# Optimization experiments

Hardware: AMD Instinct MI355X
Metric: run time of the kernel (lower is better)

The kernel has to match this reference:

```python
import jax, jax.numpy as jnp
import numpy as np

B, T, D, H, C, M = 128, 96, 256, 256, 8, 64
COMB = 4 * D + H  # z, z_prime, x_i, global_dynamics, h


def setup_inputs() -> dict:
    key = jax.random.key(0)
    ks = jax.random.split(key, 24)
    X = jax.random.normal(ks[0], (B, T, D), jnp.float32)
    X_last = jax.random.normal(ks[1], (B, T, D), jnp.float32)
    Mask = jax.random.bernoulli(ks[2], 0.5, (B, T, D)).astype(jnp.float32)
    Delta = jax.random.uniform(ks[3], (B, T, D), jnp.float32, 0.0, 5.0)
    X_last_b = jax.random.normal(ks[4], (B, T, D), jnp.float32)
    Delta_b = jax.random.uniform(ks[5], (B, T, D), jnp.float32, 0.0, 5.0)
    x = jnp.stack([X, X_last, Mask, Delta, X_last_b, Delta_b], axis=1)  # [B,6,T,D]
    X_mean = jax.random.normal(ks[6], (1, T, D), jnp.float32)
    clusters = jax.random.randint(ks[7], (D,), 1, C + 1, jnp.int64)
    s = 1.0 / np.sqrt(COMB)
    def U(k, shape, sc):
        return jax.random.uniform(k, shape, jnp.float32, -sc, sc)
    params = {
        'W_i': U(ks[8], (H, COMB), s), 'b_i': U(ks[9], (H,), s),
        'W_f': U(ks[10], (H, COMB), s), 'b_f': U(ks[11], (H,), s),
        'W_o': U(ks[12], (H, COMB), s), 'b_o': U(ks[13], (H,), s),
        'W_c': U(ks[14], (H, COMB), s), 'b_c': U(ks[15], (H,), s),
        'W_fc': U(ks[16], (D, H), 1.0 / np.sqrt(H)), 'b_fc': U(ks[17], (D,), 1.0 / np.sqrt(H)),
        'gz_w': U(ks[18], (D,), 1.0 / np.sqrt(D)), 'gz_b': U(ks[19], (D,), 1.0 / np.sqrt(D)),
        'gzp_w': U(ks[20], (D,), 1.0 / np.sqrt(D)), 'gzp_b': U(ks[21], (D,), 1.0 / np.sqrt(D)),
        'memory': jax.random.uniform(ks[22], (C, M, D), jnp.float32, -1.0 / np.sqrt(M), 1.0 / np.sqrt(M)),
    }
    k2 = jax.random.split(ks[23], 2)
    params['local_w'] = jax.random.uniform(k2[0], (3, D), jnp.float32, -1.0 / np.sqrt(3.0), 1.0 / np.sqrt(3.0))
    params['global_w'] = jax.random.uniform(k2[1], (C,), jnp.float32, -1.0 / np.sqrt(C), 1.0 / np.sqrt(C))
    return dict(x=x, X_mean=X_mean, clusters=clusters, **params)


def reference(x, X_mean, clusters, W_i, b_i, W_f, b_f, W_o, b_o, W_c, b_c,
              W_fc, b_fc, gz_w, gz_b, gzp_w, gzp_b, memory, local_w, global_w):
    # cluster one-hot feature masks: [C, D] (cluster ids are 1-based)
    cmask = (clusters[None, :] == jnp.arange(1, C + 1, dtype=clusters.dtype)[:, None]).astype(x.dtype)

    X, X_last, Mask, Delta, X_last_b, Delta_b = [x[:, i] for i in range(6)]  # each [B,T,D]
    xm = X_mean[0]  # [T,D]

    def step(carry, inp):
        h, c = carry
        xt, xl, xlb, m, d, db, mean = inp
        # FilterLinear with eye filter == diagonal linear; GRU-D decay
        dz = jnp.exp(-jax.nn.relu(d * gz_w + gz_b))
        dzp = jnp.exp(-jax.nn.relu(db * gzp_w + gzp_b))
        z = m * xt + (1 - m) * (dz * xl + (1 - dz) * mean)
        zp = m * xt + (1 - m) * (dzp * xlb + (1 - dzp) * mean)
        x_i = h @ W_fc.T + b_fc  # [B,D]
        local_stats = local_w[0] * z + local_w[1] * zp + local_w[2] * x_i  # [B,D]
        # per-cluster masked local stats -> memory attention
        li = local_stats[:, None, :] * cmask[None]              # [B,C,D]
        scores = jnp.einsum('cmd,bcd->bcm', memory, li)          # [B,C,M]
        s = jax.nn.softmax(scores, axis=-1)
        gd = jnp.einsum('bcm,cmd->bcd', s, memory)               # [B,C,D]
        gd = jnp.einsum('bcd,c->bd', gd, global_w)               # [B,D]
        combined = jnp.concatenate([z, zp, x_i, gd, h], axis=1)  # [B,4D+H]
        i = jax.nn.sigmoid(combined @ W_i.T + b_i)
        f = jax.nn.sigmoid(combined @ W_f.T + b_f)
        o = jax.nn.sigmoid(combined @ W_o.T + b_o)
        ct = jnp.tanh(combined @ W_c.T + b_c)
        c = f * c + i * ct
        h = o * jnp.tanh(c)
        out = h @ W_fc.T + b_fc
        return (h, c), out

    h0 = jnp.zeros((x.shape[0], H), x.dtype)
    c0 = jnp.zeros((x.shape[0], H), x.dtype)
    xs = (X.transpose(1, 0, 2), X_last.transpose(1, 0, 2), X_last_b.transpose(1, 0, 2),
          Mask.transpose(1, 0, 2), Delta.transpose(1, 0, 2), Delta_b.transpose(1, 0, 2), xm)
    _, outs = jax.lax.scan(step, (h0, c0), xs)
    return outs.transpose(1, 0, 2)  # [B,T,D]
```

## Files before the change

kernel.cpp:

```cpp
#include <hip/hip_runtime.h>
#include <hip/hip_bf16.h>
#include <hip/hip_fp16.h>
#include <cstdint>
#include <cstddef>


#define PLANE 24576
#define GRP 16

using bf16_t = __hip_bfloat16;
typedef __bf16 bf16x8 __attribute__((ext_vector_type(8)));
typedef float  f32x4  __attribute__((ext_vector_type(4)));
typedef unsigned int u32x4 __attribute__((ext_vector_type(4)));

__device__ __forceinline__ float  b2f(bf16_t v){ return __bfloat162float(v); }
__device__ __forceinline__ bf16_t f2b(float v){ return __float2bfloat16(v); }
__device__ __forceinline__ float ldF(const void* p, size_t i, int f32){
  return f32 ? ((const float*)p)[i] : b2f(((const bf16_t*)p)[i]);
}
__device__ __forceinline__ bf16x8 ld_frag(const void* p){
  union { uint4 u; bf16x8 v; } c;
  c.u = *(const uint4*)p;
  return c.v;
}
__device__ __forceinline__ f32x4 mfma_bf16(bf16x8 a, bf16x8 b, f32x4 c){
  return __builtin_amdgcn_mfma_f32_16x16x32_bf16(a, b, c, 0, 0, 0);
}

__device__ __forceinline__ u32x4 ld_cg(const void* p){
  u32x4 r;
  asm volatile("global_load_dwordx4 %0, %1, off sc0 sc1"
               : "=v"(r) : "v"(p) : "memory");
  return r;
}
__device__ __forceinline__ void st_cg(void* p, u32x4 v){
  asm volatile("global_store_dwordx4 %0, %1, off sc0 sc1"
               :: "v"(p), "v"(v) : "memory");
}
__device__ __forceinline__ int ld_flag(const int* p){
  int r;
  asm volatile("global_load_dword %0, %1, off sc0 sc1\n\ts_waitcnt vmcnt(0)"
               : "=v"(r) : "v"(p) : "memory");
  return r;
}
__device__ __forceinline__ void vm_wait0(){
  asm volatile("s_waitcnt vmcnt(0)" ::: "memory");
  __builtin_amdgcn_sched_barrier(0);
}

__global__ __launch_bounds__(64) void k_detect(
    const uint32_t* __restrict__ xu, const uint32_t* __restrict__ clu,
    int* __restrict__ flags)
{
  __shared__ int cnt[2];
  int t = threadIdx.x;
  if (t < 2) cnt[t] = 0;
  __syncthreads();
  uint32_t v = xu[2*PLANE + t];
  if (v == 0u || v == 0x3F800000u) atomicAdd(&cnt[0], 1);
  if (clu[2*t + 1] == 0u) atomicAdd(&cnt[1], 1);
  __syncthreads();
  if (t == 0){
    flags[0] = (cnt[0] >= 48) ? 1 : 0;
    flags[1] = (cnt[1] >= 60) ? 1 : 0;
  }
}

__global__ __launch_bounds__(256) void k_zero(int* __restrict__ bar){
  bar[threadIdx.x] = 0;
}

__global__ __launch_bounds__(256) void k_canon(
    const void* __restrict__ Wfc, const void* __restrict__ Xmean,
    const void* __restrict__ bfc, const void* __restrict__ localw,
    const void* __restrict__ globalw, const void* __restrict__ gzw,
    const void* __restrict__ gzb, const void* __restrict__ gzpw,
    const void* __restrict__ gzpb, const int* __restrict__ flags,
    bf16_t* __restrict__ WfcC, bf16_t* __restrict__ XmC,
    bf16_t* __restrict__ bfcC, bf16_t* __restrict__ lwC,
    bf16_t* __restrict__ gwC, float* __restrict__ gzC)
{
  const int f32 = flags[0];
  int i = blockIdx.x*256 + threadIdx.x;
  if (i < 65536) WfcC[i] = f2b(ldF(Wfc, i, f32));
  if (i < 24576) XmC[i]  = f2b(ldF(Xmean, i, f32));
  if (i < 256)   bfcC[i] = f2b(ldF(bfc, i, f32));
  if (i < 768)   lwC[i]  = f2b(ldF(localw, i, f32));
  if (i < 8)     gwC[i]  = f2b(ldF(globalw, i, f32));
  if (i < 256){
    gzC[i]       = ldF(gzw,  i, f32);
    gzC[256 + i] = ldF(gzb,  i, f32);
    gzC[512 + i] = ldF(gzpw, i, f32);
    gzC[768 + i] = ldF(gzpb, i, f32);
  }
}

__global__ __launch_bounds__(256) void k_fold(
    const void* __restrict__ Wi, const void* __restrict__ Wf,
    const void* __restrict__ Wo, const void* __restrict__ Wc,
    const void* __restrict__ bi, const void* __restrict__ bfg,
    const void* __restrict__ bo, const void* __restrict__ bcg,
    const void* __restrict__ Wfc, const void* __restrict__ bfc,
    const int* __restrict__ flags,
    bf16_t* __restrict__ U, bf16_t* __restrict__ Uz, float* __restrict__ bias2)
{
  const int f32 = flags[0];
  int n = blockIdx.x; int g = n & 3; int j = n >> 2;
  const void* Wg = (g==0)?Wi:(g==1)?Wf:(g==2)?Wo:Wc;
  const void* bg = (g==0)?bi:(g==1)?bfg:(g==2)?bo:bcg;
  const size_t wb = (size_t)j*1280;
  int k = threadIdx.x;
  float acc = 0.f;
  for (int d=0; d<256; ++d)
    acc += ldF(Wg, wb+512+d, f32) * ldF(Wfc, (size_t)d*256+k, f32);
  U[(size_t)n*512 + k]        = f2b(acc + ldF(Wg, wb+1024+k, f32));
  U[(size_t)n*512 + 256 + k]  = f2b(ldF(Wg, wb+768+k, f32));
  Uz[(size_t)n*512 + k]       = f2b(ldF(Wg, wb+k, f32));
  Uz[(size_t)n*512 + 256 + k] = f2b(ldF(Wg, wb+256+k, f32));
  __shared__ float red[256];
  red[k] = ldF(Wg, wb+512+k, f32) * ldF(bfc, k, f32);
  __syncthreads();
  for (int s=128; s>0; s>>=1){ if (k<s) red[k]+=red[k+s]; __syncthreads(); }
  if (k==0) bias2[n] = red[0] + ldF(bg, j, f32);
}

__global__ __launch_bounds__(256) void k_foldG(
    const void* __restrict__ Wi, const void* __restrict__ Wf,
    const void* __restrict__ Wo, const void* __restrict__ Wc,
    const void* __restrict__ memory, const int* __restrict__ flags,
    bf16_t* __restrict__ G)
{
  const int f32 = flags[0];
  __shared__ float wrow[4][256];
  int j = blockIdx.x; int tid = threadIdx.x;
  const void* Wg[4] = {Wi,Wf,Wo,Wc};
  for (int g=0; g<4; ++g)
    wrow[g][tid] = ldF(Wg[g], (size_t)j*1280 + 768 + tid, f32);
  __syncthreads();
  for (int half=0; half<2; ++half){
    int cm = half*256 + tid;
    float a0=0,a1=0,a2=0,a3=0;
    for (int d=0; d<256; ++d){
      float mv = ldF(memory, (size_t)cm*256 + d, f32);
      a0 += wrow[0][d]*mv; a1 += wrow[1][d]*mv;
      a2 += wrow[2][d]*mv; a3 += wrow[3][d]*mv;
    }
    G[(size_t)(4*j+0)*512 + cm] = f2b(a0);
    G[(size_t)(4*j+1)*512 + cm] = f2b(a1);
    G[(size_t)(4*j+2)*512 + cm] = f2b(a2);
    G[(size_t)(4*j+3)*512 + cm] = f2b(a3);
  }
}

__global__ __launch_bounds__(256) void k_foldQ(
    const int* __restrict__ clusters, const void* __restrict__ memory,
    const bf16_t* __restrict__ lwC, const bf16_t* __restrict__ WfcC,
    const bf16_t* __restrict__ bfcC, const int* __restrict__ flags,
    bf16_t* __restrict__ Mem2, bf16_t* __restrict__ Qbf, float* __restrict__ qb)
{
  const int f32 = flags[0], i64 = flags[1];
  const int cm = blockIdx.x; const int c = cm >> 6;
  const int tid = threadIdx.x;
  __shared__ float ml2[256];
  __shared__ float red[256];
  int cv = i64 ? clusters[2*tid] : clusters[tid];
  float mv = (cv == c+1) ? ldF(memory, (size_t)cm*256 + tid, f32) : 0.f;
  Mem2[(size_t)cm*256 + tid] = f2b(mv);
  float m2 = mv * b2f(lwC[512 + tid]);
  ml2[tid] = m2;
  red[tid] = m2 * b2f(bfcC[tid]);
  __syncthreads();
  float acc = 0.f;
  for (int d=0; d<256; ++d)
    acc += ml2[d] * b2f(WfcC[(size_t)d*256 + tid]);
  Qbf[(size_t)cm*256 + tid] = f2b(acc);
  for (int s=128; s>0; s>>=1){ if (tid<s) red[tid]+=red[tid+s]; __syncthreads(); }
  if (tid==0) qb[cm] = red[0];
}

__global__ __launch_bounds__(256) void k_zzp(
    const void* __restrict__ x, const bf16_t* __restrict__ XmC,
    const float* __restrict__ gzC, const bf16_t* __restrict__ lwC,
    const int* __restrict__ flags,
    bf16_t* __restrict__ Zcat, bf16_t* __restrict__ Zl)
{
  const int f32 = flags[0];
  int r = blockIdx.x;
  int t = r >> 7, b = r & 127, d = threadIdx.x;
  size_t base = (size_t)b*6*PLANE + (size_t)t*256 + d;
  float xt = ldF(x, base          , f32);
  float xl = ldF(x, base +   PLANE, f32);
  float mk = ldF(x, base + 2*PLANE, f32);
  float de = ldF(x, base + 3*PLANE, f32);
  float xlb= ldF(x, base + 4*PLANE, f32);
  float deb= ldF(x, base + 5*PLANE, f32);
  float mean = b2f(XmC[t*256+d]);
  float dz  = expf(-fmaxf(0.f, de *gzC[d]     + gzC[256+d]));
  float dzp = expf(-fmaxf(0.f, deb*gzC[512+d] + gzC[768+d]));
  float z  = mk*xt + (1.f-mk)*(dz *xl  + (1.f-dz )*mean);
  float zp = mk*xt + (1.f-mk)*(dzp*xlb + (1.f-dzp)*mean);
  Zcat[(size_t)r*512 + d]       = f2b(z);
  Zcat[(size_t)r*512 + 256 + d] = f2b(zp);
  Zl[(size_t)r*256 + d] = f2b(b2f(lwC[d])*z + b2f(lwC[256+d])*zp);
}

__global__ __launch_bounds__(256) void k_zc(
    const bf16_t* __restrict__ Zcat, const bf16_t* __restrict__ Uz,
    const float* __restrict__ bias2, __half* __restrict__ zc)
{
  const int tid = threadIdx.x;
  const int w = tid>>6, l = tid&63, q=l>>4, cl=l&15;
  const int mq = w&1, nq = w>>1;
  const int m0 = blockIdx.x*128, n0 = blockIdx.y*128;
  f32x4 acc[4][4];
#pragma unroll
  for (int a=0;a<4;++a)
#pragma unroll
    for (int b2=0;b2<4;++b2) acc[a][b2] = (f32x4){0.f,0.f,0.f,0.f};
  for (int ks=0; ks<16; ++ks){
    bf16x8 av[4], bv[4];
#pragma unroll
    for (int mi=0;mi<4;++mi)
      av[mi] = ld_frag(&Zcat[(size_t)(m0+mq*64+mi*16+cl)*512 + ks*32 + q*8]);
#pragma unroll
    for (int ni=0;ni<4;++ni)
      bv[ni] = ld_frag(&Uz[(size_t)(n0+nq*64+ni*16+cl)*512 + ks*32 + q*8]);
#pragma unroll
    for (int mi=0;mi<4;++mi)
#pragma unroll
      for (int ni=0;ni<4;++ni)
        acc[mi][ni] = mfma_bf16(av[mi], bv[ni], acc[mi][ni]);
  }
#pragma unroll
  for (int mi=0;mi<4;++mi)
#pragma unroll
    for (int ni=0;ni<4;++ni)
#pragma unroll
      for (int rr=0;rr<4;++rr){
        int m = m0 + mq*64 + mi*16 + q*4 + rr;
        int n = n0 + nq*64 + ni*16 + cl;
        zc[(size_t)m*1024 + n] = __float2half(acc[mi][ni][rr] + bias2[n]);
      }
}

__global__ __launch_bounds__(256) void k_szm(
    const bf16_t* __restrict__ Zl, const bf16_t* __restrict__ Mem2,
    const float* __restrict__ qb, __half* __restrict__ SzM)
{
  const int tid = threadIdx.x;
  const int w = tid>>6, l = tid&63, q=l>>4, cl=l&15;
  const int mq = w&1, nq = w>>1;
  const int m0 = blockIdx.x*128, n0 = blockIdx.y*128;
  f32x4 acc[4][4];
#pragma unroll
  for (int a=0;a<4;++a)
#pragma unroll
    for (int b2=0;b2<4;++b2) acc[a][b2] = (f32x4){0.f,0.f,0.f,0.f};
  for (int ks=0; ks<8; ++ks){
    bf16x8 av[4], bv[4];
#pragma unroll
    for (int mi=0;mi<4;++mi)
      av[mi] = ld_frag(&Zl[(size_t)(m0+mq*64+mi*16+cl)*256 + ks*32 + q*8]);
#pragma unroll
    for (int ni=0;ni<4;++ni)
      bv[ni] = ld_frag(&Mem2[(size_t)(n0+nq*64+ni*16+cl)*256 + ks*32 + q*8]);
#pragma unroll
    for (int mi=0;mi<4;++mi)
#pragma unroll
      for (int ni=0;ni<4;++ni)
        acc[mi][ni] = mfma_bf16(av[mi], bv[ni], acc[mi][ni]);
  }
#pragma unroll
  for (int mi=0;mi<4;++mi)
#pragma unroll
    for (int ni=0;ni<4;++ni)
#pragma unroll
      for (int rr=0;rr<4;++rr){
        int m = m0 + mq*64 + mi*16 + q*4 + rr;
        int n = n0 + nq*64 + ni*16 + cl;
        SzM[(size_t)m*512 + n] = __float2half(acc[mi][ni][rr] + qb[n]);
      }
}

__global__ __launch_bounds__(256) void k_out(
    const bf16_t* __restrict__ hSeq, const bf16_t* __restrict__ WfcC,
    const bf16_t* __restrict__ bfcC, const int* __restrict__ flags,
    void* __restrict__ outv)
{
  const int f32 = flags[0];
  const int tid = threadIdx.x;
  const int w = tid>>6, l = tid&63, q=l>>4, cl=l&15;
  const int mq = w&1, nq = w>>1;
  const int m0 = blockIdx.x*128, n0 = blockIdx.y*128;
  f32x4 acc[4][4];
#pragma unroll
  for (int a=0;a<4;++a)
#pragma unroll
    for (int b2=0;b2<4;++b2) acc[a][b2] = (f32x4){0.f,0.f,0.f,0.f};
  for (int ks=0; ks<8; ++ks){
    bf16x8 av[4], bv[4];
#pragma unroll
    for (int mi=0;mi<4;++mi)
      av[mi] = ld_frag(&hSeq[(size_t)(128 + m0+mq*64+mi*16+cl)*256 + ks*32 + q*8]);
#pragma unroll
    for (int ni=0;ni<4;++ni)
      bv[ni] = ld_frag(&WfcC[(size_t)(n0+nq*64+ni*16+cl)*256 + ks*32 + q*8]);
#pragma unroll
    for (int mi=0;mi<4;++mi)
#pragma unroll
      for (int ni=0;ni<4;++ni)
        acc[mi][ni] = mfma_bf16(av[mi], bv[ni], acc[mi][ni]);
  }
#pragma unroll
  for (int mi=0;mi<4;++mi)
#pragma unroll
    for (int ni=0;ni<4;++ni)
#pragma unroll
      for (int rr=0;rr<4;++rr){
        int m = m0 + mq*64 + mi*16 + q*4 + rr;
        int n = n0 + nq*64 + ni*16 + cl;
        float v = acc[mi][ni][rr] + b2f(bfcC[n]);
        int b = m & 127, tt = m >> 7;
        size_t ob = ((size_t)b*96 + tt)*256 + n;
        if (f32) ((float*)outv)[ob] = v; else ((bf16_t*)outv)[ob] = f2b(v);
      }
}

__global__ __launch_bounds__(256) void k_main(
    const bf16_t* __restrict__ gwC,
    const bf16_t* __restrict__ U, const bf16_t* __restrict__ G,
    const bf16_t* __restrict__ Qbf,
    const __half* __restrict__ zc, const __half* __restrict__ SzM,
    bf16_t* __restrict__ hSeq, bf16_t* __restrict__ tSeq,
    int* __restrict__ bar)
{
  __shared__ bf16_t Us[64][264];
  __shared__ bf16_t Gs[64][520];
  __shared__ bf16_t Qs[64][264];
  __shared__ bf16_t hS[16][264];
  __shared__ bf16_t tS[16][520];
  __shared__ bf16_t hO[16][16];
  __shared__ bf16_t tO[16][64];
  __shared__ float redmx[4][16];
  __shared__ float redsm[4][16];

  const int tid = threadIdx.x;
  const int W = tid>>6, l = tid&63, q = l>>4, cl = l&15;
  const int g = blockIdx.x & 7, s = blockIdx.x >> 3;
  const int r0 = g*16;
  const int n0 = s*64;
  int* barp = bar + g*32;

  for (int i=tid; i<64*32; i+=256){ int r=i>>5, c8=(i&31)*8;
    *(uint4*)(&Us[r][c8]) = *(const uint4*)(U + (size_t)(n0+r)*512 + c8); }
  for (int i=tid; i<64*64; i+=256){ int r=i>>6, c8=(i&63)*8;
    *(uint4*)(&Gs[r][c8]) = *(const uint4*)(G + (size_t)(n0+r)*512 + c8); }
  if (s<8)
    for (int i=tid; i<64*32; i+=256){ int r=i>>5, c8=(i&31)*8;
      *(uint4*)(&Qs[r][c8]) = *(const uint4*)(Qbf + (size_t)(s*64+r)*256 + c8); }
  for (int i=tid; i<16*264; i+=256) hS[i/264][i%264] = f2b(0.f);
  const float gw_c = (s<8)? b2f(gwC[s]) : 0.f;
  float creg[4] = {0.f,0.f,0.f,0.f};
  __syncthreads();

  for (int t=0; t<96; ++t){
    f32x4 acc;
#pragma unroll
    for (int rr=0; rr<4; ++rr)
      acc[rr] = __half2float(zc[((size_t)(t*128)+r0+q*4+rr)*1024 + n0 + W*16 + cl]);
    f32x4 sa = {0.f,0.f,0.f,0.f};
    if (s<8){
#pragma unroll
      for (int rr=0; rr<4; ++rr)
        sa[rr] = __half2float(SzM[((size_t)(t*128)+r0+q*4+rr)*512 + s*64 + W*16 + cl]);
    }
    if (t>0){
      if (tid==0){ while (ld_flag(barp+0) < GRP*t) {} }
      __syncthreads();
      const bf16_t* hsrc = hSeq + (size_t)t*128*256;
      u32x4 a0 = ld_cg(hsrc + (size_t)(r0 + (tid>>5))*256 + (tid&31)*8);
      u32x4 a1 = ld_cg(hsrc + (size_t)(r0 + 8 + (tid>>5))*256 + (tid&31)*8);
      vm_wait0();
      *(u32x4*)(&hS[tid>>5][(tid&31)*8]) = a0;
      *(u32x4*)(&hS[8 + (tid>>5)][(tid&31)*8]) = a1;
      __syncthreads();
    }
    if (s<8){
#pragma unroll
      for (int ks=0; ks<8; ++ks){
        bf16x8 a = ld_frag(&hS[cl][ks*32 + q*8]);
        bf16x8 b = ld_frag(&Qs[W*16+cl][ks*32 + q*8]);
        sa = mfma_bf16(a, b, sa);
      }
#pragma unroll
      for (int rr=0; rr<4; ++rr){
        float m = sa[rr];
        m = fmaxf(m, __shfl_xor(m,1));
        m = fmaxf(m, __shfl_xor(m,2));
        m = fmaxf(m, __shfl_xor(m,4));
        m = fmaxf(m, __shfl_xor(m,8));
        if (cl==0) redmx[W][q*4+rr] = m;
      }
      __syncthreads();
      float e4[4];
#pragma unroll
      for (int rr=0; rr<4; ++rr){
        int row = q*4+rr;
        float mx = fmaxf(fmaxf(redmx[0][row],redmx[1][row]),
                         fmaxf(redmx[2][row],redmx[3][row]));
        float e = expf(sa[rr]-mx);
        e4[rr] = e;
        float ss = e;
        ss += __shfl_xor(ss,1); ss += __shfl_xor(ss,2);
        ss += __shfl_xor(ss,4); ss += __shfl_xor(ss,8);
        if (cl==0) redsm[W][row] = ss;
      }
      __syncthreads();
#pragma unroll
      for (int rr=0; rr<4; ++rr){
        int row = q*4+rr;
        float sm = redsm[0][row]+redsm[1][row]+redsm[2][row]+redsm[3][row];
        tO[row][W*16 + cl] = f2b(e4[rr]*gw_c/sm);
      }
      __syncthreads();
      if (tid < 128){
        int r = tid>>3, c8 = (tid&7)*8;
        u32x4 v = *(u32x4*)(&tO[r][c8]);
        st_cg(tSeq + (size_t)t*128*512 + (size_t)(r0+r)*512 + s*64 + c8, v);
      }
      vm_wait0();
      __syncthreads();
      if (tid==0) atomicAdd(barp+16, 1);
    }
#pragma unroll
    for (int ks=0; ks<8; ++ks){
      bf16x8 a = ld_frag(&hS[cl][ks*32 + q*8]);
      bf16x8 b = ld_frag(&Us[W*16+cl][ks*32 + q*8]);
      acc = mfma_bf16(a, b, acc);
    }
    if (tid==0){ while (ld_flag(barp+16) < 8*(t+1)) {} }
    __syncthreads();
    {
      const bf16_t* tsrc = tSeq + (size_t)t*128*512;
      u32x4 b0 = ld_cg(tsrc + (size_t)(r0 + (tid>>6)     )*512 + (tid&63)*8);
      u32x4 b1 = ld_cg(tsrc + (size_t)(r0 + (tid>>6) +  4)*512 + (tid&63)*8);
      u32x4 b2 = ld_cg(tsrc + (size_t)(r0 + (tid>>6) +  8)*512 + (tid&63)*8);
      u32x4 b3 = ld_cg(tsrc + (size_t)(r0 + (tid>>6) + 12)*512 + (tid&63)*8);
      vm_wait0();
      *(u32x4*)(&tS[(tid>>6)     ][(tid&63)*8]) = b0;
      *(u32x4*)(&tS[(tid>>6) +  4][(tid&63)*8]) = b1;
      *(u32x4*)(&tS[(tid>>6) +  8][(tid&63)*8]) = b2;
      *(u32x4*)(&tS[(tid>>6) + 12][(tid&63)*8]) = b3;
      __syncthreads();
    }
#pragma unroll
    for (int ks=0; ks<16; ++ks){
      bf16x8 a = ld_frag(&tS[cl][ks*32 + q*8]);
      bf16x8 b = ld_frag(&Gs[W*16+cl][ks*32 + q*8]);
      acc = mfma_bf16(a, b, acc);
    }
    const int base = l & ~3;
#pragma unroll
    for (int rr=0; rr<4; ++rr){
      float p = acc[rr];
      float pi = __shfl(p, base+0);
      float pf = __shfl(p, base+1);
      float po = __shfl(p, base+2);
      float pc = __shfl(p, base+3);
      float iv = 1.f/(1.f+expf(-pi));
      float fv = 1.f/(1.f+expf(-pf));
      float ov = 1.f/(1.f+expf(-po));
      float cv = tanhf(pc);
      float cn = fv*creg[rr] + iv*cv;
      creg[rr] = cn;
      float hv = ov * tanhf(cn);
      if ((l&3)==0)
        hO[q*4+rr][W*4 + (cl>>2)] = f2b(hv);
    }
    __syncthreads();
    if (tid < 32){
      int r = tid>>1, c8 = (tid&1)*8;
      u32x4 v = *(u32x4*)(&hO[r][c8]);
      st_cg(hSeq + (size_t)(t+1)*128*256 + (size_t)(r0+r)*256 + s*16 + c8, v);
    }
    vm_wait0();
    __syncthreads();
    if (tid==0) atomicAdd(barp+0, 1);
  }
}

extern "C" void kernel_launch(void* const* d_in, const int* in_sizes, int n_in,
                              void* d_out, int out_size, void* d_ws, size_t ws_size,
                              hipStream_t stream)
{
  const void* x       = d_in[0];
  const void* Xmean   = d_in[1];
  const int*  clusters= (const int*)d_in[2];
  const void* Wi  = d_in[3];
  const void* bi  = d_in[4];
  const void* Wf  = d_in[5];
  const void* bfp = d_in[6];
  const void* Wo  = d_in[7];
  const void* bo  = d_in[8];
  const void* Wc  = d_in[9];
  const void* bcp = d_in[10];
  const void* Wfc = d_in[11];
  const void* bfc = d_in[12];
  const void* gzw = d_in[13];
  const void* gzb = d_in[14];
  const void* gzpw= d_in[15];
  const void* gzpb= d_in[16];
  const void* memory = d_in[17];
  const void* localw = d_in[18];
  const void* globalw= d_in[19];
  (void)in_sizes; (void)n_in; (void)out_size; (void)ws_size;

  char* ws = (char*)d_ws;
  size_t off = 0;
  auto take = [&](size_t bytes)->char*{
    char* p = ws + off; off = (off + bytes + 255) & ~(size_t)255; return p; };
  int*    flags  = (int*)   take(16);
  int*    bar    = (int*)   take(256*4);
  bf16_t* U      = (bf16_t*)take((size_t)1024*512*2);
  bf16_t* Uz     = (bf16_t*)take((size_t)1024*512*2);
  bf16_t* G      = (bf16_t*)take((size_t)1024*512*2);
  bf16_t* WfcC   = (bf16_t*)take((size_t)65536*2);
  bf16_t* XmC    = (bf16_t*)take((size_t)24576*2);
  bf16_t* bfcC   = (bf16_t*)take(256*2);
  bf16_t* lwC    = (bf16_t*)take(768*2);
  bf16_t* gwC    = (bf16_t*)take(8*2);
  float*  gzC    = (float*) take(1024*4);
  float*  bias2  = (float*) take(1024*4);
  bf16_t* Mem2   = (bf16_t*)take((size_t)512*256*2);
  bf16_t* Qbf    = (bf16_t*)take((size_t)512*256*2);
  float*  qb     = (float*) take(512*4);
  __half* zc     = (__half*)take((size_t)12288*1024*2);
  __half* SzM    = (__half*)take((size_t)12288*512*2);
  char* bigA = take((size_t)12288*512*2);
  char* bigB = take((size_t)97*128*256*2);
  bf16_t* Zcat = (bf16_t*)bigA;
  bf16_t* tSeq = (bf16_t*)bigA;
  bf16_t* Zl   = (bf16_t*)bigB;
  bf16_t* hSeq = (bf16_t*)bigB;

  k_detect<<<1,    64, 0,stream>>>((const uint32_t*)x, (const uint32_t*)clusters, flags);
  k_zero  <<<1,    256,0,stream>>>(bar);
  k_canon <<<256,  256,0,stream>>>(Wfc, Xmean, bfc, localw, globalw,
                                   gzw, gzb, gzpw, gzpb, flags,
                                   WfcC, XmC, bfcC, lwC, gwC, gzC);
  k_fold  <<<1024, 256,0,stream>>>(Wi,Wf,Wo,Wc, bi,bfp,bo,bcp, Wfc,bfc, flags,
                                   U, Uz, bias2);
  k_foldG <<<256,  256,0,stream>>>(Wi,Wf,Wo,Wc, memory, flags, G);
  k_foldQ <<<512,  256,0,stream>>>(clusters, memory, lwC, WfcC, bfcC, flags,
                                   Mem2, Qbf, qb);
  k_zzp   <<<12288,256,0,stream>>>(x, XmC, gzC, lwC, flags, Zcat, Zl);
  k_zc    <<<dim3(96,8),256,0,stream>>>(Zcat, Uz, bias2, zc);
  k_szm   <<<dim3(96,4),256,0,stream>>>(Zl, Mem2, qb, SzM);
  k_main  <<<128,  256,0,stream>>>(gwC, U, G, Qbf, zc, SzM, hSeq, tSeq, bar);
  k_out   <<<dim3(96,2),256,0,stream>>>(hSeq, WfcC, bfcC, flags, d_out);
}
```

Before: 1.047 ms.

## Replace block barriers and atomic counters with per-wave flag sync in recurrent kernel

The persistent recurrent kernel drops its shared-memory staging and __syncthreads-based step synchronisation. Each wave now polls an array of per-wave step flags (one flag per producer wave) and loads h and softmax-weight fragments straight from global memory into registers for the MFMAs. The memory-attention softmax is computed by a single wave per cluster block using shuffles instead of a cross-wave shared-memory reduction, and outputs are written as scalar stores. This is meant to shorten the per-timestep critical path of the recurrence, at the cost of more polling traffic, uncoalesced 16-bit stores, and less parallelism in the softmax stage.

```diff
diff --git a/kernel.cpp b/kernel.cpp
--- a/kernel.cpp
+++ b/kernel.cpp
@@ -6,7 +6,6 @@
 
 
 #define PLANE 24576
-#define GRP 16
 
 using bf16_t = __hip_bfloat16;
 typedef __bf16 bf16x8 __attribute__((ext_vector_type(8)));
@@ -22,6 +21,9 @@
   union { uint4 u; bf16x8 v; } c;
   c.u = *(const uint4*)p;
   return c.v;
+}
+__device__ __forceinline__ bf16x8 u2b(u32x4 u){
+  union { u32x4 u; bf16x8 v; } c; c.u = u; return c.v;
 }
 __device__ __forceinline__ f32x4 mfma_bf16(bf16x8 a, bf16x8 b, f32x4 c){
   return __builtin_amdgcn_mfma_f32_16x16x32_bf16(a, b, c, 0, 0, 0);
@@ -33,8 +35,14 @@
                : "=v"(r) : "v"(p) : "memory");
   return r;
 }
-__device__ __forceinline__ void st_cg(void* p, u32x4 v){
-  asm volatile("global_store_dwordx4 %0, %1, off sc0 sc1"
+__device__ __forceinline__ void st_cg_b16(bf16_t* p, bf16_t v){
+  union { bf16_t b; unsigned short u; } c; c.b = v;
+  int iv = (int)c.u;
+  asm volatile("global_store_short %0, %1, off sc0 sc1"
+               :: "v"(p), "v"(iv) : "memory");
+}
+__device__ __forceinline__ void st_flag(int* p, int v){
+  asm volatile("global_store_dword %0, %1, off sc0 sc1"
                :: "v"(p), "v"(v) : "memory");
 }
 __device__ __forceinline__ int ld_flag(const int* p){
@@ -67,7 +75,7 @@
 }
 
 __global__ __launch_bounds__(256) void k_zero(int* __restrict__ bar){
-  bar[threadIdx.x] = 0;
+  bar[blockIdx.x*256 + threadIdx.x] = 0;
 }
 
 __global__ __launch_bounds__(256) void k_canon(
@@ -337,19 +345,14 @@
   __shared__ bf16_t Us[64][264];
   __shared__ bf16_t Gs[64][520];
   __shared__ bf16_t Qs[64][264];
-  __shared__ bf16_t hS[16][264];
-  __shared__ bf16_t tS[16][520];
-  __shared__ bf16_t hO[16][16];
-  __shared__ bf16_t tO[16][64];
-  __shared__ float redmx[4][16];
-  __shared__ float redsm[4][16];
 
   const int tid = threadIdx.x;
   const int W = tid>>6, l = tid&63, q = l>>4, cl = l&15;
   const int g = blockIdx.x & 7, s = blockIdx.x >> 3;
   const int r0 = g*16;
   const int n0 = s*64;
-  int* barp = bar + g*32;
+  int* barA = bar + g*128;
+  int* barB = bar + g*128 + 64;
 
   for (int i=tid; i<64*32; i+=256){ int r=i>>5, c8=(i&31)*8;
     *(uint4*)(&Us[r][c8]) = *(const uint4*)(U + (size_t)(n0+r)*512 + c8); }
@@ -358,108 +361,91 @@
   if (s<8)
     for (int i=tid; i<64*32; i+=256){ int r=i>>5, c8=(i&31)*8;
       *(uint4*)(&Qs[r][c8]) = *(const uint4*)(Qbf + (size_t)(s*64+r)*256 + c8); }
-  for (int i=tid; i<16*264; i+=256) hS[i/264][i%264] = f2b(0.f);
   const float gw_c = (s<8)? b2f(gwC[s]) : 0.f;
+  const bool sc_wave = (s<8) && (W==0);
   float creg[4] = {0.f,0.f,0.f,0.f};
   __syncthreads();
 
   for (int t=0; t<96; ++t){
+    if (t>0){
+      const int* fp = barA + (l & 63);
+      int v;
+      do { int f = ld_flag(fp); v = f; } while (__any(v < t));
+    }
     f32x4 acc;
 #pragma unroll
     for (int rr=0; rr<4; ++rr)
       acc[rr] = __half2float(zc[((size_t)(t*128)+r0+q*4+rr)*1024 + n0 + W*16 + cl]);
-    f32x4 sa = {0.f,0.f,0.f,0.f};
-    if (s<8){
-#pragma unroll
-      for (int rr=0; rr<4; ++rr)
-        sa[rr] = __half2float(SzM[((size_t)(t*128)+r0+q*4+rr)*512 + s*64 + W*16 + cl]);
-    }
+    f32x4 sa[4];
+    if (sc_wave){
+#pragma unroll
+      for (int nt=0; nt<4; ++nt)
+#pragma unroll
+        for (int rr=0; rr<4; ++rr)
+          sa[nt][rr] = __half2float(
+            SzM[((size_t)(t*128)+r0+q*4+rr)*512 + s*64 + nt*16 + cl]);
+    }
+    u32x4 hu[8];
     if (t>0){
-      if (tid==0){ while (ld_flag(barp+0) < GRP*t) {} }
-      __syncthreads();
-      const bf16_t* hsrc = hSeq + (size_t)t*128*256;
-      u32x4 a0 = ld_cg(hsrc + (size_t)(r0 + (tid>>5))*256 + (tid&31)*8);
-      u32x4 a1 = ld_cg(hsrc + (size_t)(r0 + 8 + (tid>>5))*256 + (tid&31)*8);
+      const bf16_t* hsrc = hSeq + (size_t)t*128*256 + (size_t)(r0+cl)*256 + q*8;
+#pragma unroll
+      for (int ks=0; ks<8; ++ks) hu[ks] = ld_cg(hsrc + ks*32);
       vm_wait0();
-      *(u32x4*)(&hS[tid>>5][(tid&31)*8]) = a0;
-      *(u32x4*)(&hS[8 + (tid>>5)][(tid&31)*8]) = a1;
-      __syncthreads();
-    }
-    if (s<8){
+    } else {
+#pragma unroll
+      for (int ks=0; ks<8; ++ks) hu[ks] = (u32x4){0,0,0,0};
+    }
+    if (sc_wave){
 #pragma unroll
       for (int ks=0; ks<8; ++ks){
-        bf16x8 a = ld_frag(&hS[cl][ks*32 + q*8]);
-        bf16x8 b = ld_frag(&Qs[W*16+cl][ks*32 + q*8]);
-        sa = mfma_bf16(a, b, sa);
+        bf16x8 a = u2b(hu[ks]);
+#pragma unroll
+        for (int nt=0; nt<4; ++nt)
+          sa[nt] = mfma_bf16(a, ld_frag(&Qs[nt*16+cl][ks*32 + q*8]), sa[nt]);
       }
+      bf16_t* tdst = tSeq + (size_t)t*128*512 + (size_t)r0*512 + s*64;
 #pragma unroll
       for (int rr=0; rr<4; ++rr){
-        float m = sa[rr];
-        m = fmaxf(m, __shfl_xor(m,1));
-        m = fmaxf(m, __shfl_xor(m,2));
-        m = fmaxf(m, __shfl_xor(m,4));
-        m = fmaxf(m, __shfl_xor(m,8));
-        if (cl==0) redmx[W][q*4+rr] = m;
-      }
-      __syncthreads();
-      float e4[4];
-#pragma unroll
-      for (int rr=0; rr<4; ++rr){
-        int row = q*4+rr;
-        float mx = fmaxf(fmaxf(redmx[0][row],redmx[1][row]),
-                         fmaxf(redmx[2][row],redmx[3][row]));
-        float e = expf(sa[rr]-mx);
-        e4[rr] = e;
-        float ss = e;
-        ss += __shfl_xor(ss,1); ss += __shfl_xor(ss,2);
-        ss += __shfl_xor(ss,4); ss += __shfl_xor(ss,8);
-        if (cl==0) redsm[W][row] = ss;
-      }
-      __syncthreads();
-#pragma unroll
-      for (int rr=0; rr<4; ++rr){
-        int row = q*4+rr;
-        float sm = redsm[0][row]+redsm[1][row]+redsm[2][row]+redsm[3][row];
-        tO[row][W*16 + cl] = f2b(e4[rr]*gw_c/sm);
-      }
-      __syncthreads();
-      if (tid < 128){
-        int r = tid>>3, c8 = (tid&7)*8;
-        u32x4 v = *(u32x4*)(&tO[r][c8]);
-        st_cg(tSeq + (size_t)t*128*512 + (size_t)(r0+r)*512 + s*64 + c8, v);
+        float mx = fmaxf(fmaxf(sa[0][rr],sa[1][rr]), fmaxf(sa[2][rr],sa[3][rr]));
+        mx = fmaxf(mx, __shfl_xor(mx,1));
+        mx = fmaxf(mx, __shfl_xor(mx,2));
+        mx = fmaxf(mx, __shfl_xor(mx,4));
+        mx = fmaxf(mx, __shfl_xor(mx,8));
+        float e0=expf(sa[0][rr]-mx), e1=expf(sa[1][rr]-mx);
+        float e2=expf(sa[2][rr]-mx), e3=expf(sa[3][rr]-mx);
+        float sm = e0+e1+e2+e3;
+        sm += __shfl_xor(sm,1); sm += __shfl_xor(sm,2);
+        sm += __shfl_xor(sm,4); sm += __shfl_xor(sm,8);
+        float sc = gw_c/sm;
+        bf16_t* rp = tdst + (size_t)(q*4+rr)*512;
+        st_cg_b16(rp +  0 + cl, f2b(e0*sc));
+        st_cg_b16(rp + 16 + cl, f2b(e1*sc));
+        st_cg_b16(rp + 32 + cl, f2b(e2*sc));
+        st_cg_b16(rp + 48 + cl, f2b(e3*sc));
       }
       vm_wait0();
-      __syncthreads();
-      if (tid==0) atomicAdd(barp+16, 1);
-    }
-#pragma unroll
-    for (int ks=0; ks<8; ++ks){
-      bf16x8 a = ld_frag(&hS[cl][ks*32 + q*8]);
-      bf16x8 b = ld_frag(&Us[W*16+cl][ks*32 + q*8]);
-      acc = mfma_bf16(a, b, acc);
-    }
-    if (tid==0){ while (ld_flag(barp+16) < 8*(t+1)) {} }
-    __syncthreads();
+      if (l==0) st_flag(barB + s, t+1);
+    }
+#pragma unroll
+    for (int ks=0; ks<8; ++ks)
+      acc = mfma_bf16(u2b(hu[ks]), ld_frag(&Us[W*16+cl][ks*32 + q*8]), acc);
     {
-      const bf16_t* tsrc = tSeq + (size_t)t*128*512;
-      u32x4 b0 = ld_cg(tsrc + (size_t)(r0 + (tid>>6)     )*512 + (tid&63)*8);
-      u32x4 b1 = ld_cg(tsrc + (size_t)(r0 + (tid>>6) +  4)*512 + (tid&63)*8);
-      u32x4 b2 = ld_cg(tsrc + (size_t)(r0 + (tid>>6) +  8)*512 + (tid&63)*8);
-      u32x4 b3 = ld_cg(tsrc + (size_t)(r0 + (tid>>6) + 12)*512 + (tid&63)*8);
+      const int* fp = barB + (l & 7);
+      int v;
+      do { int f = ld_flag(fp); v = (l<8)? f : 0x7fffffff; } while (__any(v < t+1));
+    }
+    u32x4 tu[16];
+    {
+      const bf16_t* tsrc = tSeq + (size_t)t*128*512 + (size_t)(r0+cl)*512 + q*8;
+#pragma unroll
+      for (int ks=0; ks<16; ++ks) tu[ks] = ld_cg(tsrc + ks*32);
       vm_wait0();
-      *(u32x4*)(&tS[(tid>>6)     ][(tid&63)*8]) = b0;
-      *(u32x4*)(&tS[(tid>>6) +  4][(tid&63)*8]) = b1;
-      *(u32x4*)(&tS[(tid>>6) +  8][(tid&63)*8]) = b2;
-      *(u32x4*)(&tS[(tid>>6) + 12][(tid&63)*8]) = b3;
-      __syncthreads();
-    }
-#pragma unroll
-    for (int ks=0; ks<16; ++ks){
-      bf16x8 a = ld_frag(&tS[cl][ks*32 + q*8]);
-      bf16x8 b = ld_frag(&Gs[W*16+cl][ks*32 + q*8]);
-      acc = mfma_bf16(a, b, acc);
-    }
+    }
+#pragma unroll
+    for (int ks=0; ks<16; ++ks)
+      acc = mfma_bf16(u2b(tu[ks]), ld_frag(&Gs[W*16+cl][ks*32 + q*8]), acc);
     const int base = l & ~3;
+    bf16_t* hdst = hSeq + (size_t)(t+1)*128*256;
 #pragma unroll
     for (int rr=0; rr<4; ++rr){
       float p = acc[rr];
@@ -475,17 +461,10 @@
       creg[rr] = cn;
       float hv = ov * tanhf(cn);
       if ((l&3)==0)
-        hO[q*4+rr][W*4 + (cl>>2)] = f2b(hv);
-    }
-    __syncthreads();
-    if (tid < 32){
-      int r = tid>>1, c8 = (tid&1)*8;
-      u32x4 v = *(u32x4*)(&hO[r][c8]);
-      st_cg(hSeq + (size_t)(t+1)*128*256 + (size_t)(r0+r)*256 + s*16 + c8, v);
+        st_cg_b16(hdst + (size_t)(r0+q*4+rr)*256 + s*16 + W*4 + (cl>>2), f2b(hv));
     }
     vm_wait0();
-    __syncthreads();
-    if (tid==0) atomicAdd(barp+0, 1);
+    if (l==0) st_flag(barA + s*4 + W, t+1);
   }
 }
 
@@ -520,7 +499,7 @@
   auto take = [&](size_t bytes)->char*{
     char* p = ws + off; off = (off + bytes + 255) & ~(size_t)255; return p; };
   int*    flags  = (int*)   take(16);
-  int*    bar    = (int*)   take(256*4);
+  int*    bar    = (int*)   take(1024*4);
   bf16_t* U      = (bf16_t*)take((size_t)1024*512*2);
   bf16_t* Uz     = (bf16_t*)take((size_t)1024*512*2);
   bf16_t* G      = (bf16_t*)take((size_t)1024*512*2);
@@ -544,7 +523,7 @@
   bf16_t* hSeq = (bf16_t*)bigB;
 
   k_detect<<<1,    64, 0,stream>>>((const uint32_t*)x, (const uint32_t*)clusters, flags);
-  k_zero  <<<1,    256,0,stream>>>(bar);
+  k_zero  <<<4,    256,0,stream>>>(bar);
   k_canon <<<256,  256,0,stream>>>(Wfc, Xmean, bfc, localw, globalw,
                                    gzw, gzb, gzpw, gzpb, flags,
                                    WfcC, XmC, bfcC, lwC, gwC, gzC);
```

Measured after the change: 1.715 ms. +63.9%, slower.
